# Optimization experiments

Measured on AMD Instinct MI355X. Metric: run time of the kernel, lower is better.

Reference implementation:

```python
import jax, jax.numpy as jnp
import numpy as np

# ---- DTCWT filter banks ----------------------------------------------------
# Level-1 biorthogonal analysis filters ('near_sym_a', (5,7)-tap)
H0O = np.array([-0.05, 0.25, 0.5, 0.25, -0.05], dtype=np.float64)
H1O = np.array([-3., 15., 73., -170., 73., 15., -3.], dtype=np.float64) / 280.0
# Level>=2 quarter-shift orthogonal 10-tap Q-shift analysis filters
H0B = np.array([0.03516384, 0.0, -0.08832942, 0.23389032, 0.76027237,
                0.58751830, 0.0, -0.11430184, 0.0, 0.0], dtype=np.float64)
H0A = H0B[::-1].copy()
H1A = H0B * ((-1.0) ** np.arange(10))
H1B = H1A[::-1].copy()

_SQRT_HALF = float(np.sqrt(0.5))


def _reflect(x, minx, maxx):
    # dtcwt-style symmetric reflection of sample indices about half-sample edges
    rng = maxx - minx
    mod = np.fmod(x - minx, 2.0 * rng)
    mod = np.where(mod < 0, mod + 2.0 * rng, mod)
    out = np.where(mod >= rng, 2.0 * rng - mod, mod) + minx
    return np.round(out).astype(np.int64)


def _conv_valid(xe, h):
    # 'valid' convolution (np.convolve convention) along the last axis,
    # written as a static sum of shifted slices (filters are tiny)
    m = len(h)
    L = xe.shape[-1] - m + 1
    out = None
    for k in range(m):
        hk = float(h[k])
        if hk == 0.0:
            continue
        term = hk * xe[..., m - 1 - k: m - 1 - k + L]
        out = term if out is None else out + term
    return out


def colfilter(x, h, axis):
    # level-1 size-preserving FIR filter with symmetric edge extension
    x = jnp.moveaxis(x, axis, -1)
    m2 = len(h) // 2
    pad = [(0, 0)] * (x.ndim - 1) + [(m2, m2)]
    y = _conv_valid(jnp.pad(x, pad, mode='symmetric'), h)
    return jnp.moveaxis(y, -1, axis)


def coldfilt(x, ha, hb, axis):
    # dtcwt 'coldfilt': decimate-by-2 dual-tree Q-shift filtering
    x = jnp.moveaxis(x, axis, -1)
    r = x.shape[-1]
    m = len(ha)
    xe = x[..., _reflect(np.arange(-m, r + m), -0.5, r - 0.5)]
    t = np.arange(5, r + 2 * m - 2, 4)
    ya = _conv_valid(xe[..., t - 1], ha[0::2]) + _conv_valid(xe[..., t - 3], ha[1::2])
    yb = _conv_valid(xe[..., t], hb[0::2]) + _conv_valid(xe[..., t - 2], hb[1::2])
    pair = [ya, yb] if float(np.sum(ha * hb)) > 0 else [yb, ya]
    y = jnp.stack(pair, axis=-1).reshape(x.shape[:-1] + (r // 2,))
    return jnp.moveaxis(y, -1, axis)


def q2c(y):
    # quads of real samples -> two complex subbands, as (real, imag) pairs
    a, b = y[:, 0::2, 0::2], y[:, 0::2, 1::2]
    c, d = y[:, 1::2, 0::2], y[:, 1::2, 1::2]
    return (((a - d) * _SQRT_HALF, (b + c) * _SQRT_HALF),
            ((a + d) * _SQRT_HALF, (b - c) * _SQRT_HALF))


def _bands(hi_lo, lo_hi, hi_hi):
    # dtcwt orientation order: [0,5]<-Hi*h0, [2,3]<-Lo*h1, [1,4]<-Hi*h1
    (r0, i0), (r5, i5) = q2c(hi_lo)
    (r2, i2), (r3, i3) = q2c(lo_hi)
    (r1, i1), (r4, i4) = q2c(hi_hi)
    real = jnp.stack([r0, r1, r2, r3, r4, r5], axis=-1)  # (B,H',W',C,6)
    imag = jnp.stack([i0, i1, i2, i3, i4, i5], axis=-1)
    return real, imag


def dtcwt_forward(x):
    # x: (B,H,W,C) nhwc; 2-level 2D DTCWT applied per channel
    lo = colfilter(x, H0O, 1)
    hi = colfilter(x, H1O, 1)
    lolo = colfilter(lo, H0O, 2)
    re0, im0 = _bands(colfilter(hi, H0O, 2), colfilter(lo, H1O, 2),
                      colfilter(hi, H1O, 2))
    lo2 = coldfilt(lolo, H0B, H0A, 1)
    hi2 = coldfilt(lolo, H1B, H1A, 1)
    lolo2 = coldfilt(lo2, H0B, H0A, 2)
    re1, im1 = _bands(coldfilt(hi2, H0B, H0A, 2), coldfilt(lo2, H1B, H1A, 2),
                      coldfilt(hi2, H1B, H1A, 2))
    B, H2, W2, C, _ = re0.shape
    # high0 channel order from the layer: (is_imag, channel i, orientation j)
    out_h0 = jnp.stack([re0, im0], axis=3).reshape(B, H2, W2, 2 * C * 6)
    # high1 channel order from the layer: (is_imag, orientation j, channel i)
    B, H4, W4, _, _ = re1.shape
    out_h1 = jnp.stack([jnp.moveaxis(re1, -1, -2), jnp.moveaxis(im1, -1, -2)],
                       axis=3).reshape(B, H4, W4, 2 * 6 * C)
    return lolo2, out_h0, out_h1


def setup_inputs() -> dict:
    key = jax.random.key(0)
    x = jax.random.normal(key, (16, 512, 512, 3), dtype=jnp.float32)
    return {"x": x}


def reference(x):
    return dtcwt_forward(x)
```

## Files before the change

### kernel.cpp

```cpp
#include <hip/hip_runtime.h>

#define SQH 0.70710678118654752440f

typedef float nf4 __attribute__((ext_vector_type(4)));
__device__ __forceinline__ void nt_store4(float4 v, float4* p) {
  __builtin_nontemporal_store(__builtin_bit_cast(nf4, v), (nf4*)p);
}

namespace dt {
constexpr float H0Oh[3] = {-0.05f, 0.25f, 0.5f};
constexpr float H1Oh[4] = {-3.f/280.f, 15.f/280.f, 73.f/280.f, -170.f/280.f};
constexpr float H0Os[3] = {-0.05f*SQH, 0.25f*SQH, 0.5f*SQH};
constexpr float H1Os[4] = {(-3.f/280.f)*SQH, (15.f/280.f)*SQH,
                           (73.f/280.f)*SQH, (-170.f/280.f)*SQH};
constexpr float H0B[10] = {0.03516384f, 0.f, -0.08832942f, 0.23389032f, 0.76027237f,
                           0.5875183f, 0.f, -0.11430184f, 0.f, 0.f};
constexpr float H0A[10] = {0.f, 0.f, -0.11430184f, 0.f, 0.5875183f,
                           0.76027237f, 0.23389032f, -0.08832942f, 0.f, 0.03516384f};
constexpr float H1A[10] = {0.03516384f, 0.f, -0.08832942f, -0.23389032f, 0.76027237f,
                           -0.5875183f, 0.f, 0.11430184f, 0.f, 0.f};
constexpr float H1B[10] = {0.f, 0.f, 0.11430184f, 0.f, -0.5875183f,
                           0.76027237f, -0.23389032f, -0.08832942f, 0.f, 0.03516384f};
}

__device__ __forceinline__ int refl512(int i) {
  i = (i < 0) ? (-1 - i) : i;
  return (i > 511) ? (1023 - i) : i;
}

__device__ __forceinline__ unsigned int packh2(float a, float b) {
  const unsigned short ua = __builtin_bit_cast(unsigned short, (_Float16)a);
  const unsigned short ub = __builtin_bit_cast(unsigned short, (_Float16)b);
  return (unsigned int)ua | ((unsigned int)ub << 16);
}
__device__ __forceinline__ unsigned short f2h(float a) {
  return __builtin_bit_cast(unsigned short, (_Float16)a);
}
__device__ __forceinline__ float h2f(unsigned short u) {
  return (float)__builtin_bit_cast(_Float16, u);
}
__device__ __forceinline__ float4 h4tof4(ushort4 v) {
  return make_float4(h2f(v.x), h2f(v.y), h2f(v.z), h2f(v.w));
}
__device__ __forceinline__ float2 u2f2(unsigned int u) {
  return make_float2(h2f((unsigned short)(u & 0xffff)),
                     h2f((unsigned short)(u >> 16)));
}

__global__ __launch_bounds__(384)
void k_level1(const float* __restrict__ x, unsigned short* __restrict__ lolo,
              float* __restrict__ outh0) {
  const int flat = blockIdx.x + (blockIdx.y << 4) + (blockIdx.z << 8);
  const int tile = ((flat & 7) << 9) + (flat >> 3);
  const int b  = tile >> 8;
  const int h0 = ((tile >> 4) & 15) << 5;
  const int w0 = (tile & 15) << 5;
  const int t  = threadIdx.x;

  __shared__ float s_lo[3 * 656];
  __shared__ float s_hi[3 * 656];
  __shared__ float s_pack[4608];

  const int q = t & 127;
  const int g = t >> 7;
  const bool hact = (q < 114) && (g < 2);
  const float* xc = nullptr;
  int pbase = 0;
  {
    int cw = q / 3, cch = q - 3 * (q / 3);
    if (q >= 114) { cw = 37; cch = 0; }
    xc = x + (size_t)b * 786432 + refl512(w0 - 3 + cw) * 3 + cch;
    pbase = cch * 656 + (8 * (g & 1)) * 40 + cw;
  }

  auto hload = [&](int h, float* v) {
    if (!hact) return;
    const int rb = h0 + 16 * h + 8 * g - 3;
#pragma unroll
    for (int rr = 0; rr < 14; ++rr)
      v[rr] = xc[(size_t)refl512(rb + rr) * 1536];
  };
  auto hfilt = [&](const float* v) {
    if (!hact) return;
    float* plo = s_lo + pbase;
    float* phi = s_hi + pbase;
#pragma unroll
    for (int rr = 0; rr < 8; ++rr) {
      plo[rr*40] = dt::H0Oh[0]*(v[rr+1]+v[rr+5]) + dt::H0Oh[1]*(v[rr+2]+v[rr+4])
                 + dt::H0Oh[2]*v[rr+3];
      phi[rr*40] = dt::H1Oh[0]*(v[rr]+v[rr+6]) + dt::H1Oh[1]*(v[rr+1]+v[rr+5])
                 + dt::H1Oh[2]*(v[rr+2]+v[rr+4]) + dt::H1Oh[3]*v[rr+3];
    }
  };

  const int c   = t % 3;
  const int jq  = (t / 3) & 15;
  const int rp0 = t / 48;
  const int lobase = c * 656 + 2 * jq;
  float* pk = s_pack + rp0 * 576 + jq * 36 + c * 6;

  auto quadphase = [&]() -> float4 {
    const int r0 = rp0 << 1;
    float G0[10], G1[10];
    {
      const float2* d = (const float2*)(s_hi + lobase + r0 * 40);
      const float2* e = (const float2*)(s_hi + lobase + r0 * 40 + 40);
#pragma unroll
      for (int u = 0; u < 5; ++u) {
        float2 vd = d[u]; G0[2*u] = vd.x; G0[2*u+1] = vd.y;
        float2 ve = e[u]; G1[2*u] = ve.x; G1[2*u+1] = ve.y;
      }
    }
    const float hl00 = dt::H0Os[0]*(G0[1]+G0[5]) + dt::H0Os[1]*(G0[2]+G0[4]) + dt::H0Os[2]*G0[3];
    const float hl01 = dt::H0Os[0]*(G0[2]+G0[6]) + dt::H0Os[1]*(G0[3]+G0[5]) + dt::H0Os[2]*G0[4];
    const float hl10 = dt::H0Os[0]*(G1[1]+G1[5]) + dt::H0Os[1]*(G1[2]+G1[4]) + dt::H0Os[2]*G1[3];
    const float hl11 = dt::H0Os[0]*(G1[2]+G1[6]) + dt::H0Os[1]*(G1[3]+G1[5]) + dt::H0Os[2]*G1[4];
    const float hh00 = dt::H1Os[0]*(G0[0]+G0[6]) + dt::H1Os[1]*(G0[1]+G0[5]) + dt::H1Os[2]*(G0[2]+G0[4]) + dt::H1Os[3]*G0[3];
    const float hh01 = dt::H1Os[0]*(G0[1]+G0[7]) + dt::H1Os[1]*(G0[2]+G0[6]) + dt::H1Os[2]*(G0[3]+G0[5]) + dt::H1Os[3]*G0[4];
    const float hh10 = dt::H1Os[0]*(G1[0]+G1[6]) + dt::H1Os[1]*(G1[1]+G1[5]) + dt::H1Os[2]*(G1[2]+G1[4]) + dt::H1Os[3]*G1[3];
    const float hh11 = dt::H1Os[0]*(G1[1]+G1[7]) + dt::H1Os[1]*(G1[2]+G1[6]) + dt::H1Os[2]*(G1[3]+G1[5]) + dt::H1Os[3]*G1[4];
    pk[0]  = hl00 - hl11;  pk[18] = hl01 + hl10;
    pk[5]  = hl00 + hl11;  pk[23] = hl01 - hl10;
    pk[1]  = hh00 - hh11;  pk[19] = hh01 + hh10;
    pk[4]  = hh00 + hh11;  pk[22] = hh01 - hh10;
    float L0[10], L1[10];
    {
      const float2* a  = (const float2*)(s_lo + lobase + r0 * 40);
      const float2* bq = (const float2*)(s_lo + lobase + r0 * 40 + 40);
#pragma unroll
      for (int u = 0; u < 5; ++u) {
        float2 va = a[u];  L0[2*u] = va.x; L0[2*u+1] = va.y;
        float2 vb = bq[u]; L1[2*u] = vb.x; L1[2*u+1] = vb.y;
      }
    }
    const float lh00 = dt::H1Os[0]*(L0[0]+L0[6]) + dt::H1Os[1]*(L0[1]+L0[5]) + dt::H1Os[2]*(L0[2]+L0[4]) + dt::H1Os[3]*L0[3];
    const float lh01 = dt::H1Os[0]*(L0[1]+L0[7]) + dt::H1Os[1]*(L0[2]+L0[6]) + dt::H1Os[2]*(L0[3]+L0[5]) + dt::H1Os[3]*L0[4];
    const float lh10 = dt::H1Os[0]*(L1[0]+L1[6]) + dt::H1Os[1]*(L1[1]+L1[5]) + dt::H1Os[2]*(L1[2]+L1[4]) + dt::H1Os[3]*L1[3];
    const float lh11 = dt::H1Os[0]*(L1[1]+L1[7]) + dt::H1Os[1]*(L1[2]+L1[6]) + dt::H1Os[2]*(L1[3]+L1[5]) + dt::H1Os[3]*L1[4];
    pk[2]  = lh00 - lh11;  pk[20] = lh01 + lh10;
    pk[3]  = lh00 + lh11;  pk[21] = lh01 - lh10;
    float4 ll;
    ll.x = dt::H0Oh[0]*(L0[1]+L0[5]) + dt::H0Oh[1]*(L0[2]+L0[4]) + dt::H0Oh[2]*L0[3];
    ll.y = dt::H0Oh[0]*(L0[2]+L0[6]) + dt::H0Oh[1]*(L0[3]+L0[5]) + dt::H0Oh[2]*L0[4];
    ll.z = dt::H0Oh[0]*(L1[1]+L1[5]) + dt::H0Oh[1]*(L1[2]+L1[4]) + dt::H0Oh[2]*L1[3];
    ll.w = dt::H0Oh[0]*(L1[2]+L1[6]) + dt::H0Oh[1]*(L1[3]+L1[5]) + dt::H0Oh[2]*L1[4];
    return ll;
  };

  const float4* sp4 = (const float4*)s_pack;
  auto storePack = [&](int h, float4 f0, float4 f1, float4 f2) {
    const int gi0 = (h0 >> 1) + (h << 3);
    float4* gout = (float4*)(outh0 + ((((size_t)b << 8) + gi0) << 8) * 36
                             + (size_t)(w0 >> 1) * 36);
    { const int it = t;       nt_store4(f0, &gout[(size_t)(it/144) * 2304 + (it%144)]); }
    { const int it = t + 384; nt_store4(f1, &gout[(size_t)(it/144) * 2304 + (it%144)]); }
    { const int it = t + 768; nt_store4(f2, &gout[(size_t)(it/144) * 2304 + (it%144)]); }
  };

  float v0[14], v1[14];
  hload(0, v0);
  hfilt(v0);
  __syncthreads();
  hload(1, v1);
  const float4 llA = quadphase();
  __syncthreads();
  float4 f0 = sp4[t], f1 = sp4[t + 384], f2 = sp4[t + 768];
  hfilt(v1);
  __syncthreads();
  storePack(0, f0, f1, f2);
  const float4 llB = quadphase();
  __syncthreads();
  f0 = sp4[t]; f1 = sp4[t + 384]; f2 = sp4[t + 768];
  storePack(1, f0, f1, f2);
  {
    unsigned short* lp = lolo + (((size_t)(b * 3 + c) * 512) + (h0 + (rp0 << 1))) * 512
                         + w0 + 2 * jq;
    *(unsigned int*)lp              = packh2(llA.x, llA.y);
    *(unsigned int*)(lp + 512)      = packh2(llA.z, llA.w);
    *(unsigned int*)(lp + 16 * 512) = packh2(llB.x, llB.y);
    *(unsigned int*)(lp + 17 * 512) = packh2(llB.z, llB.w);
  }
}

#define SM(s, c, r, p) (((((s)*3 + (c))*4 + (r))*2 + (p)) * 266)

__global__ __launch_bounds__(256)
void k_level2(const unsigned short* __restrict__ lolo, float* __restrict__ out0,
              float* __restrict__ outh1) {
  const int flat = blockIdx.x;
  const int bi = ((flat & 7) << 7) + (flat >> 3);
  const int b  = bi >> 6;
  const int jb = bi & 63;
  const int t  = threadIdx.x;
  const int n0 = jb << 1;
  const int m0 = jb << 2;

  __shared__ float s_buf[9216];
  unsigned short* s_mid16 = (unsigned short*)s_buf;

  for (int k = 0; k < 3; ++k) {
    const int idx = t + (k << 8);
    const int g  = idx & 127;
    const int cc = (idx >> 7) % 3;
    const int np = idx / 384;
    const int n  = n0 + np;
    const ushort4* sp = (const ushort4*)(lolo + (size_t)(b*3+cc) * 262144) + g;
    float4 E[8], O[8];
    const int EOFF[8] = {-8, -4, -2, 0, 2, 4, 6, 10};
    const int OOFF[8] = {-7, -3, -1, 1, 3, 5, 7, 11};
#pragma unroll
    for (int u = 0; u < 8; ++u) {
      E[u] = h4tof4(sp[(size_t)refl512(4*n + EOFF[u]) * 128]);
      O[u] = h4tof4(sp[(size_t)refl512(4*n + OOFF[u]) * 128]);
    }
#define MAD4(acc, h, v) { acc.x += (h)*v.x; acc.y += (h)*v.y; \
                          acc.z += (h)*v.z; acc.w += (h)*v.w; }
    float4 alo  = make_float4(0.f,0.f,0.f,0.f);
    MAD4(alo,  dt::H0B[0], E[7]); MAD4(alo,  dt::H0B[2], E[6]);
    MAD4(alo,  dt::H0B[3], E[5]); MAD4(alo,  dt::H0B[4], E[4]);
    MAD4(alo,  dt::H0B[5], E[3]); MAD4(alo,  dt::H0B[7], E[1]);
    float4 ahi  = make_float4(0.f,0.f,0.f,0.f);
    MAD4(ahi,  dt::H1A[0], O[7]); MAD4(ahi,  dt::H1A[2], O[6]);
    MAD4(ahi,  dt::H1A[3], O[5]); MAD4(ahi,  dt::H1A[4], O[4]);
    MAD4(ahi,  dt::H1A[5], O[3]); MAD4(ahi,  dt::H1A[7], O[1]);
    float4 alo2 = make_float4(0.f,0.f,0.f,0.f);
    MAD4(alo2, dt::H0A[2], O[6]); MAD4(alo2, dt::H0A[4], O[4]);
    MAD4(alo2, dt::H0A[5], O[3]); MAD4(alo2, dt::H0A[6], O[2]);
    MAD4(alo2, dt::H0A[7], O[1]); MAD4(alo2, dt::H0A[9], O[0]);
    float4 ahi2 = make_float4(0.f,0.f,0.f,0.f);
    MAD4(ahi2, dt::H1B[2], E[6]); MAD4(ahi2, dt::H1B[4], E[4]);
    MAD4(ahi2, dt::H1B[5], E[3]); MAD4(ahi2, dt::H1B[6], E[2]);
    MAD4(ahi2, dt::H1B[7], E[1]); MAD4(ahi2, dt::H1B[9], E[0]);
#undef MAD4
    const int me = np << 1, mo = me + 1;
    *(unsigned int*)&s_mid16[SM(0,cc,me,0) + 2*g + 4] = packh2(alo.x,  alo.z);
    *(unsigned int*)&s_mid16[SM(0,cc,me,1) + 2*g + 4] = packh2(alo.y,  alo.w);
    *(unsigned int*)&s_mid16[SM(1,cc,me,0) + 2*g + 4] = packh2(ahi.x,  ahi.z);
    *(unsigned int*)&s_mid16[SM(1,cc,me,1) + 2*g + 4] = packh2(ahi.y,  ahi.w);
    *(unsigned int*)&s_mid16[SM(0,cc,mo,0) + 2*g + 4] = packh2(alo2.x, alo2.z);
    *(unsigned int*)&s_mid16[SM(0,cc,mo,1) + 2*g + 4] = packh2(alo2.y, alo2.w);
    *(unsigned int*)&s_mid16[SM(1,cc,mo,0) + 2*g + 4] = packh2(ahi2.x, ahi2.z);
    *(unsigned int*)&s_mid16[SM(1,cc,mo,1) + 2*g + 4] = packh2(ahi2.y, ahi2.w);
  }

  {
    const int mi  = t >> 6;
    const int rem = t & 63;
    if (rem < 48) {
      const int cc = rem >> 4;
      const int hc = rem & 15;
      const int w  = (hc < 8) ? (hc - 8) : (504 + hc);
      const int u  = w >> 1;
      const int par = w & 1;
      const int wc = refl512(w);
      const int n  = n0 + (mi >> 1);
      const unsigned short* sp = lolo + (size_t)(b*3+cc) * 262144 + wc;
      float alo = 0.f, ahi = 0.f;
      if ((mi & 1) == 0) {
#pragma unroll
        for (int q = 0; q < 10; ++q) {
          if (dt::H0B[q] != 0.f) alo += dt::H0B[q] * h2f(sp[(size_t)refl512(4*n+10-2*q)*512]);
          if (dt::H1A[q] != 0.f) ahi += dt::H1A[q] * h2f(sp[(size_t)refl512(4*n+11-2*q)*512]);
        }
      } else {
#pragma unroll
        for (int q = 0; q < 10; ++q) {
          if (dt::H0A[q] != 0.f) alo += dt::H0A[q] * h2f(sp[(size_t)refl512(4*n+11-2*q)*512]);
          if (dt::H1B[q] != 0.f) ahi += dt::H1B[q] * h2f(sp[(size_t)refl512(4*n+10-2*q)*512]);
        }
      }
      s_mid16[SM(0,cc,mi,par) + u + 4] = f2h(alo);
      s_mid16[SM(1,cc,mi,par) + u + 4] = f2h(ahi);
    }
  }
  __syncthreads();

  float roh[3][12];
#pragma unroll
  for (int k = 0; k < 3; ++k) {
    const int idx = t + (k << 8);
    const int cc = idx % 3;
    const int jj = (idx / 3) & 127;
    const int rp = idx / 384;
    const int base0 = 2 * jj;

    float q_hl[2][2], q_hh[2][2], q_lh[2][2];
#pragma unroll
    for (int r = 0; r < 2; ++r) {
      const int mi = (rp << 1) + r;
      float el[10], ol[10], eh[10], oh[10];
#pragma unroll
      for (int u = 0; u < 5; ++u) {
        const float2 w0v = u2f2(*(const unsigned int*)&s_mid16[SM(0,cc,mi,0) + base0 + 2*u]);
        el[2*u] = w0v.x; el[2*u+1] = w0v.y;
        const float2 w1v = u2f2(*(const unsigned int*)&s_mid16[SM(0,cc,mi,1) + base0 + 2*u]);
        ol[2*u] = w1v.x; ol[2*u+1] = w1v.y;
        const float2 w2v = u2f2(*(const unsigned int*)&s_mid16[SM(1,cc,mi,0) + base0 + 2*u]);
        eh[2*u] = w2v.x; eh[2*u+1] = w2v.y;
        const float2 w3v = u2f2(*(const unsigned int*)&s_mid16[SM(1,cc,mi,1) + base0 + 2*u]);
        oh[2*u] = w3v.x; oh[2*u+1] = w3v.y;
      }
      float ll_e = 0.f, ll_o = 0.f, hl_e = 0.f, hl_o = 0.f;
      float lh_e = 0.f, lh_o = 0.f, hh_e = 0.f, hh_o = 0.f;
#pragma unroll
      for (int q = 0; q < 10; ++q) {
        if (dt::H0B[q] != 0.f) { ll_e += dt::H0B[q]*el[9-q]; hl_e += dt::H0B[q]*eh[9-q]; }
        if (dt::H0A[q] != 0.f) { ll_o += dt::H0A[q]*ol[9-q]; hl_o += dt::H0A[q]*oh[9-q]; }
        if (dt::H1A[q] != 0.f) { lh_e += dt::H1A[q]*ol[9-q]; hh_e += dt::H1A[q]*oh[9-q]; }
        if (dt::H1B[q] != 0.f) { lh_o += dt::H1B[q]*el[9-q]; hh_o += dt::H1B[q]*eh[9-q]; }
      }
      float* o0 = out0 + (((size_t)(b << 8) + (m0 + mi)) * 256 + 2*jj) * 3 + cc;
      __builtin_nontemporal_store(ll_e, o0);
      __builtin_nontemporal_store(ll_o, o0 + 3);
      q_hl[r][0] = hl_e; q_hl[r][1] = hl_o;
      q_hh[r][0] = hh_e; q_hh[r][1] = hh_o;
      q_lh[r][0] = lh_e; q_lh[r][1] = lh_o;
    }
    roh[k][0]  = SQH * (q_hl[0][0] - q_hl[1][1]);
    roh[k][1]  = SQH * (q_hl[0][1] + q_hl[1][0]);
    roh[k][2]  = SQH * (q_hl[0][0] + q_hl[1][1]);
    roh[k][3]  = SQH * (q_hl[0][1] - q_hl[1][0]);
    roh[k][4]  = SQH * (q_hh[0][0] - q_hh[1][1]);
    roh[k][5]  = SQH * (q_hh[0][1] + q_hh[1][0]);
    roh[k][6]  = SQH * (q_hh[0][0] + q_hh[1][1]);
    roh[k][7]  = SQH * (q_hh[0][1] - q_hh[1][0]);
    roh[k][8]  = SQH * (q_lh[0][0] - q_lh[1][1]);
    roh[k][9]  = SQH * (q_lh[0][1] + q_lh[1][0]);
    roh[k][10] = SQH * (q_lh[0][0] + q_lh[1][1]);
    roh[k][11] = SQH * (q_lh[0][1] - q_lh[1][0]);
  }
  __syncthreads();

#pragma unroll
  for (int k = 0; k < 3; ++k) {
    const int idx = t + (k << 8);
    const int cc = idx % 3;
    const int jj = (idx / 3) & 127;
    const int rp = idx / 384;
    float* ph = s_buf + rp * 4608 + jj * 36 + cc;
    ph[0]  = roh[k][0];  ph[18] = roh[k][1];
    ph[15] = roh[k][2];  ph[33] = roh[k][3];
    ph[3]  = roh[k][4];  ph[21] = roh[k][5];
    ph[12] = roh[k][6];  ph[30] = roh[k][7];
    ph[6]  = roh[k][8];  ph[24] = roh[k][9];
    ph[9]  = roh[k][10]; ph[27] = roh[k][11];
  }
  __syncthreads();

  const float4* sm4 = (const float4*)s_buf;
  float4* d1 = (float4*)(outh1 + (size_t)(b * 128 + 2 * jb) * 4608);
#pragma unroll
  for (int j = 0; j < 9; ++j)
    nt_store4(sm4[t + j * 256], &d1[t + j * 256]);
}

extern "C" void kernel_launch(void* const* d_in, const int* in_sizes, int n_in,
                              void* d_out, int out_size, void* d_ws, size_t ws_size,
                              hipStream_t stream) {
  const float* x = (const float*)d_in[0];
  float* out = (float*)d_out;

  float* out0  = out;
  float* outh0 = out + 3145728;
  float* outh1 = out + 40894464;

  unsigned short* lolo = (unsigned short*)d_ws;

  k_level1<<<dim3(16, 16, 16), 384, 0, stream>>>(x, lolo, outh0);
  k_level2<<<1024, 256, 0, stream>>>(lolo, out0, outh1);
}
```

Measured before the change: 60.68 us.

## Halve level-2 block work to one output row pair, doubling grid size

Each level-2 block now handles one decimated row group (one n) instead of two, so the grid doubles to 2048 blocks and shared memory per block halves. The edge-column pass is rebalanced so each of 192 threads computes a single filtered value rather than two. The aim is more parallelism and occupancy in the second kernel, at the cost of fewer threads doing useful work per block (384 items over 256 threads leaves idle lanes) and more per-block overhead.

```diff
diff --git a/kernel.cpp b/kernel.cpp
--- a/kernel.cpp
+++ b/kernel.cpp
@@ -182,28 +182,26 @@
   }
 }
 
-#define SM(s, c, r, p) (((((s)*3 + (c))*4 + (r))*2 + (p)) * 266)
+#define SM2(s, c, mi, p) (((((s)*3 + (c))*2 + (mi))*2 + (p)) * 266)
 
 __global__ __launch_bounds__(256)
 void k_level2(const unsigned short* __restrict__ lolo, float* __restrict__ out0,
               float* __restrict__ outh1) {
   const int flat = blockIdx.x;
-  const int bi = ((flat & 7) << 7) + (flat >> 3);
-  const int b  = bi >> 6;
-  const int jb = bi & 63;
-  const int t  = threadIdx.x;
-  const int n0 = jb << 1;
-  const int m0 = jb << 2;
-
-  __shared__ float s_buf[9216];
+  const int bi = ((flat & 7) << 8) + (flat >> 3);
+  const int b   = bi >> 7;
+  const int jb2 = bi & 127;
+  const int t   = threadIdx.x;
+  const int n   = jb2;
+
+  __shared__ float s_buf[4608];
   unsigned short* s_mid16 = (unsigned short*)s_buf;
 
-  for (int k = 0; k < 3; ++k) {
+  for (int k = 0; k < 2; ++k) {
     const int idx = t + (k << 8);
+    if (idx >= 384) break;
     const int g  = idx & 127;
-    const int cc = (idx >> 7) % 3;
-    const int np = idx / 384;
-    const int n  = n0 + np;
+    const int cc = idx >> 7;
     const ushort4* sp = (const ushort4*)(lolo + (size_t)(b*3+cc) * 262144) + g;
     float4 E[8], O[8];
     const int EOFF[8] = {-8, -4, -2, 0, 2, 4, 6, 10};
@@ -232,84 +230,92 @@
     MAD4(ahi2, dt::H1B[5], E[3]); MAD4(ahi2, dt::H1B[6], E[2]);
     MAD4(ahi2, dt::H1B[7], E[1]); MAD4(ahi2, dt::H1B[9], E[0]);
 #undef MAD4
-    const int me = np << 1, mo = me + 1;
-    *(unsigned int*)&s_mid16[SM(0,cc,me,0) + 2*g + 4] = packh2(alo.x,  alo.z);
-    *(unsigned int*)&s_mid16[SM(0,cc,me,1) + 2*g + 4] = packh2(alo.y,  alo.w);
-    *(unsigned int*)&s_mid16[SM(1,cc,me,0) + 2*g + 4] = packh2(ahi.x,  ahi.z);
-    *(unsigned int*)&s_mid16[SM(1,cc,me,1) + 2*g + 4] = packh2(ahi.y,  ahi.w);
-    *(unsigned int*)&s_mid16[SM(0,cc,mo,0) + 2*g + 4] = packh2(alo2.x, alo2.z);
-    *(unsigned int*)&s_mid16[SM(0,cc,mo,1) + 2*g + 4] = packh2(alo2.y, alo2.w);
-    *(unsigned int*)&s_mid16[SM(1,cc,mo,0) + 2*g + 4] = packh2(ahi2.x, ahi2.z);
-    *(unsigned int*)&s_mid16[SM(1,cc,mo,1) + 2*g + 4] = packh2(ahi2.y, ahi2.w);
-  }
-
-  {
-    const int mi  = t >> 6;
-    const int rem = t & 63;
-    if (rem < 48) {
-      const int cc = rem >> 4;
-      const int hc = rem & 15;
-      const int w  = (hc < 8) ? (hc - 8) : (504 + hc);
-      const int u  = w >> 1;
-      const int par = w & 1;
-      const int wc = refl512(w);
-      const int n  = n0 + (mi >> 1);
-      const unsigned short* sp = lolo + (size_t)(b*3+cc) * 262144 + wc;
-      float alo = 0.f, ahi = 0.f;
-      if ((mi & 1) == 0) {
-#pragma unroll
-        for (int q = 0; q < 10; ++q) {
-          if (dt::H0B[q] != 0.f) alo += dt::H0B[q] * h2f(sp[(size_t)refl512(4*n+10-2*q)*512]);
-          if (dt::H1A[q] != 0.f) ahi += dt::H1A[q] * h2f(sp[(size_t)refl512(4*n+11-2*q)*512]);
-        }
+    *(unsigned int*)&s_mid16[SM2(0,cc,0,0) + 2*g + 4] = packh2(alo.x,  alo.z);
+    *(unsigned int*)&s_mid16[SM2(0,cc,0,1) + 2*g + 4] = packh2(alo.y,  alo.w);
+    *(unsigned int*)&s_mid16[SM2(1,cc,0,0) + 2*g + 4] = packh2(ahi.x,  ahi.z);
+    *(unsigned int*)&s_mid16[SM2(1,cc,0,1) + 2*g + 4] = packh2(ahi.y,  ahi.w);
+    *(unsigned int*)&s_mid16[SM2(0,cc,1,0) + 2*g + 4] = packh2(alo2.x, alo2.z);
+    *(unsigned int*)&s_mid16[SM2(0,cc,1,1) + 2*g + 4] = packh2(alo2.y, alo2.w);
+    *(unsigned int*)&s_mid16[SM2(1,cc,1,0) + 2*g + 4] = packh2(ahi2.x, ahi2.z);
+    *(unsigned int*)&s_mid16[SM2(1,cc,1,1) + 2*g + 4] = packh2(ahi2.y, ahi2.w);
+  }
+
+  if (t < 192) {
+    const int pl = t >> 4;
+    const int s  = t & 15;
+    const int src = pl / 6;
+    const int rem = pl - 6 * src;
+    const int cc  = rem >> 1;
+    const int mi  = rem & 1;
+    const int par = s >> 3;
+    const int s3  = s & 7;
+    const int u   = (s3 < 4) ? (s3 - 4) : (252 + s3);
+    const int w   = 2 * u + par;
+    const int wc  = refl512(w);
+    const unsigned short* sp = lolo + (size_t)(b*3+cc) * 262144 + wc;
+    float acc = 0.f;
+    if (mi == 0) {
+      if (src == 0) {
+#pragma unroll
+        for (int qq = 0; qq < 10; ++qq)
+          if (dt::H0B[qq] != 0.f) acc += dt::H0B[qq] * h2f(sp[(size_t)refl512(4*n+10-2*qq)*512]);
       } else {
 #pragma unroll
-        for (int q = 0; q < 10; ++q) {
-          if (dt::H0A[q] != 0.f) alo += dt::H0A[q] * h2f(sp[(size_t)refl512(4*n+11-2*q)*512]);
-          if (dt::H1B[q] != 0.f) ahi += dt::H1B[q] * h2f(sp[(size_t)refl512(4*n+10-2*q)*512]);
-        }
-      }
-      s_mid16[SM(0,cc,mi,par) + u + 4] = f2h(alo);
-      s_mid16[SM(1,cc,mi,par) + u + 4] = f2h(ahi);
-    }
-  }
-  __syncthreads();
-
-  float roh[3][12];
-#pragma unroll
-  for (int k = 0; k < 3; ++k) {
+        for (int qq = 0; qq < 10; ++qq)
+          if (dt::H1A[qq] != 0.f) acc += dt::H1A[qq] * h2f(sp[(size_t)refl512(4*n+11-2*qq)*512]);
+      }
+    } else {
+      if (src == 0) {
+#pragma unroll
+        for (int qq = 0; qq < 10; ++qq)
+          if (dt::H0A[qq] != 0.f) acc += dt::H0A[qq] * h2f(sp[(size_t)refl512(4*n+11-2*qq)*512]);
+      } else {
+#pragma unroll
+        for (int qq = 0; qq < 10; ++qq)
+          if (dt::H1B[qq] != 0.f) acc += dt::H1B[qq] * h2f(sp[(size_t)refl512(4*n+10-2*qq)*512]);
+      }
+    }
+    s_mid16[SM2(src,cc,mi,par) + u + 4] = f2h(acc);
+  }
+  __syncthreads();
+
+  float roh[2][12];
+  bool act2[2] = {false, false};
+#pragma unroll
+  for (int k = 0; k < 2; ++k) {
     const int idx = t + (k << 8);
+    if (idx >= 384) break;
+    act2[k] = true;
     const int cc = idx % 3;
-    const int jj = (idx / 3) & 127;
-    const int rp = idx / 384;
+    const int jj = idx / 3;
     const int base0 = 2 * jj;
 
     float q_hl[2][2], q_hh[2][2], q_lh[2][2];
 #pragma unroll
     for (int r = 0; r < 2; ++r) {
-      const int mi = (rp << 1) + r;
+      const int mi = r;
       float el[10], ol[10], eh[10], oh[10];
 #pragma unroll
       for (int u = 0; u < 5; ++u) {
-        const float2 w0v = u2f2(*(const unsigned int*)&s_mid16[SM(0,cc,mi,0) + base0 + 2*u]);
+        const float2 w0v = u2f2(*(const unsigned int*)&s_mid16[SM2(0,cc,mi,0) + base0 + 2*u]);
         el[2*u] = w0v.x; el[2*u+1] = w0v.y;
-        const float2 w1v = u2f2(*(const unsigned int*)&s_mid16[SM(0,cc,mi,1) + base0 + 2*u]);
+        const float2 w1v = u2f2(*(const unsigned int*)&s_mid16[SM2(0,cc,mi,1) + base0 + 2*u]);
         ol[2*u] = w1v.x; ol[2*u+1] = w1v.y;
-        const float2 w2v = u2f2(*(const unsigned int*)&s_mid16[SM(1,cc,mi,0) + base0 + 2*u]);
+        const float2 w2v = u2f2(*(const unsigned int*)&s_mid16[SM2(1,cc,mi,0) + base0 + 2*u]);
         eh[2*u] = w2v.x; eh[2*u+1] = w2v.y;
-        const float2 w3v = u2f2(*(const unsigned int*)&s_mid16[SM(1,cc,mi,1) + base0 + 2*u]);
+        const float2 w3v = u2f2(*(const unsigned int*)&s_mid16[SM2(1,cc,mi,1) + base0 + 2*u]);
         oh[2*u] = w3v.x; oh[2*u+1] = w3v.y;
       }
       float ll_e = 0.f, ll_o = 0.f, hl_e = 0.f, hl_o = 0.f;
       float lh_e = 0.f, lh_o = 0.f, hh_e = 0.f, hh_o = 0.f;
 #pragma unroll
-      for (int q = 0; q < 10; ++q) {
-        if (dt::H0B[q] != 0.f) { ll_e += dt::H0B[q]*el[9-q]; hl_e += dt::H0B[q]*eh[9-q]; }
-        if (dt::H0A[q] != 0.f) { ll_o += dt::H0A[q]*ol[9-q]; hl_o += dt::H0A[q]*oh[9-q]; }
-        if (dt::H1A[q] != 0.f) { lh_e += dt::H1A[q]*ol[9-q]; hh_e += dt::H1A[q]*oh[9-q]; }
-        if (dt::H1B[q] != 0.f) { lh_o += dt::H1B[q]*el[9-q]; hh_o += dt::H1B[q]*eh[9-q]; }
-      }
-      float* o0 = out0 + (((size_t)(b << 8) + (m0 + mi)) * 256 + 2*jj) * 3 + cc;
+      for (int qq = 0; qq < 10; ++qq) {
+        if (dt::H0B[qq] != 0.f) { ll_e += dt::H0B[qq]*el[9-qq]; hl_e += dt::H0B[qq]*eh[9-qq]; }
+        if (dt::H0A[qq] != 0.f) { ll_o += dt::H0A[qq]*ol[9-qq]; hl_o += dt::H0A[qq]*oh[9-qq]; }
+        if (dt::H1A[qq] != 0.f) { lh_e += dt::H1A[qq]*ol[9-qq]; hh_e += dt::H1A[qq]*oh[9-qq]; }
+        if (dt::H1B[qq] != 0.f) { lh_o += dt::H1B[qq]*el[9-qq]; hh_o += dt::H1B[qq]*eh[9-qq]; }
+      }
+      float* o0 = out0 + (((size_t)(b << 8) + 2*jb2 + r) * 256 + 2*jj) * 3 + cc;
       __builtin_nontemporal_store(ll_e, o0);
       __builtin_nontemporal_store(ll_o, o0 + 3);
       q_hl[r][0] = hl_e; q_hl[r][1] = hl_o;
@@ -332,12 +338,12 @@
   __syncthreads();
 
 #pragma unroll
-  for (int k = 0; k < 3; ++k) {
+  for (int k = 0; k < 2; ++k) {
+    if (!act2[k]) break;
     const int idx = t + (k << 8);
     const int cc = idx % 3;
-    const int jj = (idx / 3) & 127;
-    const int rp = idx / 384;
-    float* ph = s_buf + rp * 4608 + jj * 36 + cc;
+    const int jj = idx / 3;
+    float* ph = s_buf + jj * 36 + cc;
     ph[0]  = roh[k][0];  ph[18] = roh[k][1];
     ph[15] = roh[k][2];  ph[33] = roh[k][3];
     ph[3]  = roh[k][4];  ph[21] = roh[k][5];
@@ -348,10 +354,12 @@
   __syncthreads();
 
   const float4* sm4 = (const float4*)s_buf;
-  float4* d1 = (float4*)(outh1 + (size_t)(b * 128 + 2 * jb) * 4608);
-#pragma unroll
-  for (int j = 0; j < 9; ++j)
-    nt_store4(sm4[t + j * 256], &d1[t + j * 256]);
+  float4* d1 = (float4*)(outh1 + (size_t)(b * 128 + jb2) * 4608);
+#pragma unroll
+  for (int j = 0; j < 5; ++j) {
+    const int it = t + j * 256;
+    if (it < 1152) nt_store4(sm4[it], &d1[it]);
+  }
 }
 
 extern "C" void kernel_launch(void* const* d_in, const int* in_sizes, int n_in,
@@ -367,5 +375,5 @@
   unsigned short* lolo = (unsigned short*)d_ws;
 
   k_level1<<<dim3(16, 16, 16), 384, 0, stream>>>(x, lolo, outh0);
-  k_level2<<<1024, 256, 0, stream>>>(lolo, out0, outh1);
-}
+  k_level2<<<2048, 256, 0, stream>>>(lolo, out0, outh1);
+}
```

New measurement: 64.16 us. 1.06x slower.
